# Kernel tuning notes

Hardware: AMD Instinct MI355X
Metric: run time of the kernel (lower is better)

The kernel has to match this reference:

```python
import jax, jax.numpy as jnp
import numpy as np

E = 1024
H = 16
CH = E // H

def setup_inputs() -> dict:
    key = jax.random.key(0)
    ks = jax.random.split(key, 9)
    s = E ** -0.5
    return {
        'x': jax.random.normal(ks[0], (4, 2048, E), dtype=jnp.float32),
        'Wq': jax.random.normal(ks[1], (E, E), dtype=jnp.float32) * s,
        'bq': jnp.zeros((E,), dtype=jnp.float32),
        'Wk': jax.random.normal(ks[2], (E, E), dtype=jnp.float32) * s,
        'bk': jnp.zeros((E,), dtype=jnp.float32),
        'Wv': jax.random.normal(ks[3], (E, E), dtype=jnp.float32) * s,
        'bv': jnp.zeros((E,), dtype=jnp.float32),
        'Wo': jax.random.normal(ks[4], (E, E), dtype=jnp.float32) * s,
        'bo': jnp.zeros((E,), dtype=jnp.float32),
    }

def _split_heads(t):
    # [..., n, H*ch] -> [..., H, n, ch]
    b, n, e = t.shape
    return t.reshape(b, n, H, CH).transpose(0, 2, 1, 3)

def reference(x, Wq, bq, Wk, bk, Wv, bv, Wo, bo):
    scale = CH ** -0.5
    q = _split_heads(x @ Wq.T + bq)  # [b,H,n,ch]
    k = _split_heads(x @ Wk.T + bk)
    v = _split_heads(x @ Wv.T + bv)
    att = jnp.einsum('bhqc,bhkc->bhqk', q, k) * scale
    att = jax.nn.softmax(att, axis=-1)
    out = jnp.einsum('bhqk,bhkc->bhqc', att, v)  # [b,H,n,ch]
    b, h, n, c = out.shape
    out = out.transpose(0, 2, 1, 3).reshape(b, n, h * c)
    return out @ Wo.T + bo
```

## Files before the change

### kernel.cpp

```cpp
#include <hip/hip_runtime.h>
#include <stdint.h>

#define EMB   1024
#define NHEAD 16
#define CHD   64
#define NB    4
#define SEQ   2048
#define NTOK  (NB * SEQ)
#define KDIM  1024

typedef __attribute__((ext_vector_type(8))) short  bf16x8;
typedef __attribute__((ext_vector_type(4))) short  short4v;
typedef __attribute__((ext_vector_type(4))) float  f32x4;
typedef __attribute__((ext_vector_type(4))) float  float4v;

__device__ __forceinline__ short f2bf(float f) {
    unsigned int u = __float_as_uint(f);
    u += 0x7fffu + ((u >> 16) & 1u);
    return (short)(u >> 16);
}

__device__ __forceinline__ void async16(const short* g, short* l) {
    __builtin_amdgcn_global_load_lds((__attribute__((address_space(1))) void const*)g,
                                     (__attribute__((address_space(3))) void*)l, 16, 0, 0);
}

__global__ __launch_bounds__(256) void cvt_all(const float* __restrict__ x,
                                               const float* __restrict__ Wq,
                                               const float* __restrict__ Wk,
                                               const float* __restrict__ Wv,
                                               const float* __restrict__ Wo,
                                               short* __restrict__ xb,
                                               short* __restrict__ Wqb,
                                               short* __restrict__ Wkb,
                                               short* __restrict__ Wvb,
                                               short* __restrict__ Wob) {
    int bid = blockIdx.x;
    const float* src;
    short* dst;
    int idx;
    if (bid < 8192) {
        src = x; dst = xb; idx = bid * 256 + threadIdx.x;
    } else {
        int w  = (bid - 8192) >> 10;
        int lb = (bid - 8192) & 1023;
        src = (w == 0) ? Wq : (w == 1) ? Wk : (w == 2) ? Wv : Wo;
        dst = (w == 0) ? Wqb : (w == 1) ? Wkb : (w == 2) ? Wvb : Wob;
        idx = lb * 256 + threadIdx.x;
    }
    float4v v = ((const float4v*)src)[idx];
    short4v s;
    s.x = f2bf(v.x); s.y = f2bf(v.y); s.z = f2bf(v.z); s.w = f2bf(v.w);
    ((short4v*)dst)[idx] = s;
}

__device__ __forceinline__ void gemm_core(const short* __restrict__ Atile,
                                          const short* __restrict__ Btile,
                                          short* As, short* Bs, f32x4 acc[4][4]) {
    const int tid  = threadIdx.x;
    const int wave = tid >> 6, lane = tid & 63;
    const int quad = lane >> 4, l16 = lane & 15;
    const int wm = (wave >> 1) * 64, wn = (wave & 1) * 64;
    const int srow = lane >> 2;
    const int scol = (lane & 3) * 8;

    for (int k0 = 0; k0 < KDIM; k0 += 32) {
        __syncthreads();
#pragma unroll
        for (int c = 0; c < 2; ++c) {
            int chunk = wave * 2 + c;
            int row = chunk * 16 + srow;
            async16(Atile + (size_t)row * KDIM + k0 + scol, As + chunk * 512);
            async16(Btile + (size_t)row * KDIM + k0 + scol, Bs + chunk * 512);
        }
        __syncthreads();
        bf16x8 af[4], bfr[4];
#pragma unroll
        for (int i = 0; i < 4; ++i)
            af[i] = *(const bf16x8*)&As[(wm + i * 16 + l16) * 32 + quad * 8];
#pragma unroll
        for (int j = 0; j < 4; ++j)
            bfr[j] = *(const bf16x8*)&Bs[(wn + j * 16 + l16) * 32 + quad * 8];
#pragma unroll
        for (int i = 0; i < 4; ++i)
#pragma unroll
            for (int j = 0; j < 4; ++j)
                acc[i][j] = __builtin_amdgcn_mfma_f32_16x16x32_bf16(af[i], bfr[j], acc[i][j], 0, 0, 0);
    }
}

#define QSCALE 0.1803368801111204f


#define MFMA16(A,B,C) __builtin_amdgcn_mfma_f32_16x16x32_bf16(A,B,C,0,0,0)
#define BARR  { __builtin_amdgcn_s_barrier(); __builtin_amdgcn_sched_barrier(0); }
#define VMC4  asm volatile("s_waitcnt vmcnt(4)" ::: "memory");
#define VMC0  asm volatile("s_waitcnt vmcnt(0)" ::: "memory");
#define PRIO1 __builtin_amdgcn_s_setprio(1);
#define PRIO0 __builtin_amdgcn_s_setprio(0);

#define STAGE_A_(BUF,H,T) { \
    async16(aS0 + (size_t)(H)*131072 + (T)*64, sm + (BUF)*32768 + (H)*8192 + stA); \
    async16(aS1 + (size_t)(H)*131072 + (T)*64, sm + (BUF)*32768 + (H)*8192 + 4096 + stA); }
#define STAGE_B_(BUF,H,T) { \
    async16(bS0 + (size_t)(H)*131072 + (T)*64, sm + (BUF)*32768 + 16384 + (H)*8192 + stA); \
    async16(bS1 + (size_t)(H)*131072 + (T)*64, sm + (BUF)*32768 + 16384 + (H)*8192 + 4096 + stA); }

#define LDB_(BUF) { \
    const short* _pb = sm + (BUF)*32768 + bro; \
    bfr[0][0] = *(const bf16x8*)(_pb + ac0);        bfr[0][1] = *(const bf16x8*)(_pb + ac1); \
    bfr[1][0] = *(const bf16x8*)(_pb + 1024 + ac0); bfr[1][1] = *(const bf16x8*)(_pb + 1024 + ac1); \
    bfr[2][0] = *(const bf16x8*)(_pb + 2048 + ac0); bfr[2][1] = *(const bf16x8*)(_pb + 2048 + ac1); \
    bfr[3][0] = *(const bf16x8*)(_pb + 3072 + ac0); bfr[3][1] = *(const bf16x8*)(_pb + 3072 + ac1); }

#define LDA_(BUF,Q) { \
    const short* _pa = sm + (BUF)*32768 + aro + (Q)*2048; \
    af[0][0] = *(const bf16x8*)(_pa + ac0);        af[0][1] = *(const bf16x8*)(_pa + ac1); \
    af[1][0] = *(const bf16x8*)(_pa + 1024 + ac0); af[1][1] = *(const bf16x8*)(_pa + 1024 + ac1); }

#define MF_(Q) { \
    acc[2*(Q)][0]   = MFMA16(af[0][0], bfr[0][0], acc[2*(Q)][0]); \
    acc[2*(Q)][0]   = MFMA16(af[0][1], bfr[0][1], acc[2*(Q)][0]); \
    acc[2*(Q)][1]   = MFMA16(af[0][0], bfr[1][0], acc[2*(Q)][1]); \
    acc[2*(Q)][1]   = MFMA16(af[0][1], bfr[1][1], acc[2*(Q)][1]); \
    acc[2*(Q)][2]   = MFMA16(af[0][0], bfr[2][0], acc[2*(Q)][2]); \
    acc[2*(Q)][2]   = MFMA16(af[0][1], bfr[2][1], acc[2*(Q)][2]); \
    acc[2*(Q)][3]   = MFMA16(af[0][0], bfr[3][0], acc[2*(Q)][3]); \
    acc[2*(Q)][3]   = MFMA16(af[0][1], bfr[3][1], acc[2*(Q)][3]); \
    acc[2*(Q)+1][0] = MFMA16(af[1][0], bfr[0][0], acc[2*(Q)+1][0]); \
    acc[2*(Q)+1][0] = MFMA16(af[1][1], bfr[0][1], acc[2*(Q)+1][0]); \
    acc[2*(Q)+1][1] = MFMA16(af[1][0], bfr[1][0], acc[2*(Q)+1][1]); \
    acc[2*(Q)+1][1] = MFMA16(af[1][1], bfr[1][1], acc[2*(Q)+1][1]); \
    acc[2*(Q)+1][2] = MFMA16(af[1][0], bfr[2][0], acc[2*(Q)+1][2]); \
    acc[2*(Q)+1][2] = MFMA16(af[1][1], bfr[2][1], acc[2*(Q)+1][2]); \
    acc[2*(Q)+1][3] = MFMA16(af[1][0], bfr[3][0], acc[2*(Q)+1][3]); \
    acc[2*(Q)+1][3] = MFMA16(af[1][1], bfr[3][1], acc[2*(Q)+1][3]); }

#define WINDOW(RB, AB, TA, BB, TB) \
    LDB_(RB) LDA_(RB,0) STAGE_A_(AB,0,TA) BARR \
    PRIO1 MF_(0) PRIO0 BARR \
    LDA_(RB,1) STAGE_A_(AB,1,TA) BARR \
    PRIO1 MF_(1) PRIO0 BARR \
    LDA_(RB,2) STAGE_B_(BB,0,TB) BARR \
    PRIO1 MF_(2) PRIO0 BARR \
    LDA_(RB,3) STAGE_B_(BB,1,TB) BARR \
    PRIO1 MF_(3) PRIO0 VMC4 BARR

__global__ __launch_bounds__(512, 2) void qk256(const short* __restrict__ xb,
                                                const short* __restrict__ Wqk,
                                                const float* __restrict__ bq,
                                                const float* __restrict__ bk,
                                                short* __restrict__ Qb,
                                                short* __restrict__ Kb) {
    extern __shared__ short sm[];
    const int bm = blockIdx.x, bn = blockIdx.y;
    const int tid = threadIdx.x;
    const int w = tid >> 6, lane = tid & 63;
    const int kq = lane >> 4, l16 = lane & 15;
    const int wmi = w >> 2, wni = w & 3;

    const int colsw = ((lane & 7) * 8) ^ (((lane >> 5) & 1) << 4);
    const short* aS0 = xb  + (size_t)(bm * 256 + w * 8 + (lane >> 3)) * 1024 + colsw;
    const short* aS1 = aS0 + (size_t)64 * 1024;
    const short* bS0 = Wqk + (size_t)(bn * 256 + w * 8 + (lane >> 3)) * 1024 + colsw;
    const short* bS1 = bS0 + (size_t)64 * 1024;
    const int stA = w * 512;

    const int swz = (l16 & 4) ? 16 : 0;
    const int ac0 = (kq * 8) ^ swz;
    const int ac1 = (32 + kq * 8) ^ swz;
    const int aro = wmi * 8192 + l16 * 64;
    const int bro = 16384 + (wni >> 1) * 8192 + ((wni & 1) * 64 + l16) * 64;

    f32x4 acc[8][4];
    const f32x4 z = {0.f, 0.f, 0.f, 0.f};
#pragma unroll
    for (int m = 0; m < 8; ++m)
#pragma unroll
        for (int n = 0; n < 4; ++n) acc[m][n] = z;
    bf16x8 bfr[4][2], af[2][2];

    STAGE_A_(0,0,0) STAGE_A_(0,1,0) STAGE_B_(0,0,0) STAGE_B_(0,1,0)
    STAGE_B_(1,0,1) STAGE_B_(1,1,1)
    VMC4 BARR

    for (int it = 0; it < 7; ++it) {
        const int te = 2 * it;
        WINDOW(0, 1, te + 1, 0, te + 2)
        WINDOW(1, 0, te + 2, 1, te + 3)
    }
    LDB_(0) LDA_(0,0) STAGE_A_(1,0,15) BARR
    PRIO1 MF_(0) PRIO0 BARR
    LDA_(0,1) STAGE_A_(1,1,15) BARR
    PRIO1 MF_(1) PRIO0 BARR
    LDA_(0,2) BARR
    PRIO1 MF_(2) PRIO0 BARR
    LDA_(0,3) BARR
    PRIO1 MF_(3) PRIO0 VMC0 BARR
    LDB_(1)
    LDA_(1,0) MF_(0)
    LDA_(1,1) MF_(1)
    LDA_(1,2) MF_(2)
    LDA_(1,3) MF_(3)

    const bool isQ = (bn < 4);
    const float* bias = isQ ? bq : bk;
    short* dst = isQ ? Qb : Kb;
    const float sc = isQ ? QSCALE : 1.0f;
    const int fb = (bn & 3) * 256 + wni * 64 + l16;
    const int tok0 = bm * 256 + wmi * 128 + kq * 4;
#pragma unroll
    for (int n = 0; n < 4; ++n) {
        const int e = fb + n * 16;
        const int hh = e >> 6, cc = e & 63;
        const float bv_ = bias[e];
#pragma unroll
        for (int m = 0; m < 8; ++m)
#pragma unroll
            for (int r = 0; r < 4; ++r) {
                const int tok = tok0 + m * 16 + r;
                const int bb = tok >> 11, nn = tok & 2047;
                dst[(((size_t)bb * NHEAD + hh) * SEQ + nn) * CHD + cc] =
                    f2bf((acc[m][n][r] + bv_) * sc);
            }
    }
}

__global__ __launch_bounds__(256) void vproj(const short* __restrict__ xb,
                                             const short* __restrict__ Wvb,
                                             const float* __restrict__ bv,
                                             short* __restrict__ Vtb) {
    __shared__ short As[128 * 32], Bs[128 * 32];
    const int bm = blockIdx.x;
    const int ew = blockIdx.y * 128;

    f32x4 acc[4][4];
    const f32x4 z = {0.f, 0.f, 0.f, 0.f};
#pragma unroll
    for (int i = 0; i < 4; ++i)
#pragma unroll
        for (int j = 0; j < 4; ++j) acc[i][j] = z;

    gemm_core(Wvb + (size_t)ew * KDIM, xb + (size_t)bm * 128 * KDIM, As, Bs, acc);

    const int lane = threadIdx.x & 63, wave = threadIdx.x >> 6;
    const int quad = lane >> 4, l16 = lane & 15;
    const int wm = (wave >> 1) * 64, wn = (wave & 1) * 64;
#pragma unroll
    for (int i = 0; i < 4; ++i)
#pragma unroll
        for (int j = 0; j < 4; ++j)
#pragma unroll
            for (int r = 0; r < 4; ++r) {
                int e = ew + wm + i * 16 + quad * 4 + r;
                int token = bm * 128 + wn + j * 16 + l16;
                int bb = token >> 11, nn = token & 2047;
                int hh = e >> 6, cc = e & 63;
                Vtb[(((size_t)bb * NHEAD + hh) * CHD + cc) * SEQ + nn] =
                    f2bf(acc[i][j][r] + bv[e]);
            }
}

__global__ __launch_bounds__(256, 4) void attn(const short* __restrict__ Qb,
                                               const short* __restrict__ Kb,
                                               const short* __restrict__ Vtb,
                                               short* __restrict__ AOb) {
    __shared__ short Ks[16 * 512];
    __shared__ short Vs[16 * 512];

    const int lid = blockIdx.x;
    const int bh = (lid & 7) * 8 + (lid >> 7);
    const int qt = (lid >> 3) & 15;

    const int tid = threadIdx.x, wave = tid >> 6, lane = tid & 63;
    const int quad = lane >> 4, l16 = lane & 15;

    const short* Kg = Kb  + (size_t)bh * SEQ * CHD;
    const short* Vg = Vtb + (size_t)bh * CHD * SEQ;

    bf16x8 qf0[2], qf1[2];
#pragma unroll
    for (int g = 0; g < 2; ++g) {
        const short* Qg = Qb + ((size_t)bh * SEQ + qt * 128 + wave * 32 + g * 16 + l16) * CHD;
        qf0[g] = *(const bf16x8*)(Qg + quad * 8);
        qf1[g] = *(const bf16x8*)(Qg + 32 + quad * 8);
    }

    const int kr = lane >> 3, ku = (lane & 7) ^ kr;
    const int vr = lane >> 4, vu = (lane & 15) ^ (vr << 2);

    int koff[4], voff[4];
#pragma unroll
    for (int cc = 0; cc < 4; ++cc) {
        int c = wave * 4 + cc;
        int l = c * 8 + kr;
        int j = l >> 4, m = l & 15;
        int kvg = ((j >> 1) << 5) + ((m >> 2) << 3) + ((j & 1) << 2) + (m & 3);
        koff[cc] = kvg * CHD + ku * 8;
        voff[cc] = (c * 4 + vr) * SEQ + vu * 8;
    }

    const int krow = l16 & 7;
    const int kbase = ((l16 >> 3) * 512) + krow * 64;
    const short* kp0 = Ks + kbase + ((quad ^ krow) << 3);
    const short* kp1 = Ks + kbase + (((4 + quad) ^ krow) << 3);
    const int vrow = l16 & 3;
    const short* vp = Vs + (l16 >> 2) * 512 + vrow * 128 + quad * 8;

    const f32x4 zf = {0.f, 0.f, 0.f, 0.f};
    const bf16x8 onesv = {16256, 16256, 16256, 16256, 16256, 16256, 16256, 16256};
    f32x4 O[2][4];
#pragma unroll
    for (int g = 0; g < 2; ++g)
#pragma unroll
        for (int nb = 0; nb < 4; ++nb) O[g][nb] = zf;
    f32x4 lacc[2];
    lacc[0] = zf; lacc[1] = zf;

    const short* Kgp = Kg;
    const short* Vgp = Vg;

    for (int kt = 0; kt < 16; ++kt) {
        __syncthreads();
#pragma unroll
        for (int cc = 0; cc < 4; ++cc) {
            int c = wave * 4 + cc;
            async16(Kgp + koff[cc], Ks + c * 512);
            async16(Vgp + voff[cc], Vs + c * 512);
        }
        Kgp += 128 * CHD;
        Vgp += 128;
        __syncthreads();

#pragma unroll
        for (int kk = 0; kk < 4; ++kk) {
            bf16x8 kA0 = *(const bf16x8*)(kp0 + (2 * kk) * 1024);
            bf16x8 kA1 = *(const bf16x8*)(kp1 + (2 * kk) * 1024);
            bf16x8 kB0 = *(const bf16x8*)(kp0 + (2 * kk + 1) * 1024);
            bf16x8 kB1 = *(const bf16x8*)(kp1 + (2 * kk + 1) * 1024);

            union { int i[4]; bf16x8 v; } pf[2];
#pragma unroll
            for (int g = 0; g < 2; ++g) {
                PRIO1
                f32x4 sA = __builtin_amdgcn_mfma_f32_16x16x32_bf16(kA0, qf0[g], zf, 0, 0, 0);
                sA = __builtin_amdgcn_mfma_f32_16x16x32_bf16(kA1, qf1[g], sA, 0, 0, 0);
                f32x4 sB = __builtin_amdgcn_mfma_f32_16x16x32_bf16(kB0, qf0[g], zf, 0, 0, 0);
                sB = __builtin_amdgcn_mfma_f32_16x16x32_bf16(kB1, qf1[g], sB, 0, 0, 0);
                PRIO0

                unsigned a0 = __float_as_uint(__builtin_amdgcn_exp2f(sA.x));
                unsigned a1 = __float_as_uint(__builtin_amdgcn_exp2f(sA.y));
                unsigned a2 = __float_as_uint(__builtin_amdgcn_exp2f(sA.z));
                unsigned a3 = __float_as_uint(__builtin_amdgcn_exp2f(sA.w));
                unsigned b0 = __float_as_uint(__builtin_amdgcn_exp2f(sB.x));
                unsigned b1 = __float_as_uint(__builtin_amdgcn_exp2f(sB.y));
                unsigned b2 = __float_as_uint(__builtin_amdgcn_exp2f(sB.z));
                unsigned b3 = __float_as_uint(__builtin_amdgcn_exp2f(sB.w));
                pf[g].i[0] = __builtin_amdgcn_perm(a1, a0, 0x07060302u);
                pf[g].i[1] = __builtin_amdgcn_perm(a3, a2, 0x07060302u);
                pf[g].i[2] = __builtin_amdgcn_perm(b1, b0, 0x07060302u);
                pf[g].i[3] = __builtin_amdgcn_perm(b3, b2, 0x07060302u);

                lacc[g] = __builtin_amdgcn_mfma_f32_16x16x32_bf16(pf[g].v, onesv, lacc[g], 0, 0, 0);
            }

            const short* vpk = vp + ((kk ^ vrow) << 5);
            PRIO1
#pragma unroll
            for (int nb = 0; nb < 4; ++nb) {
                bf16x8 vf = *(const bf16x8*)(vpk + nb * 2048);
#pragma unroll
                for (int g = 0; g < 2; ++g)
                    O[g][nb] = __builtin_amdgcn_mfma_f32_16x16x32_bf16(pf[g].v, vf, O[g][nb], 0, 0, 0);
            }
            PRIO0
        }
    }

    const int b = bh >> 4, h = bh & 15;
#pragma unroll
    for (int g = 0; g < 2; ++g) {
        float linv[4];
#pragma unroll
        for (int r = 0; r < 4; ++r) linv[r] = 1.0f / lacc[g][r];
#pragma unroll
        for (int nb = 0; nb < 4; ++nb)
#pragma unroll
            for (int r = 0; r < 4; ++r) {
                int n = qt * 128 + wave * 32 + g * 16 + quad * 4 + r;
                int cc = nb * 16 + l16;
                AOb[((size_t)b * SEQ + n) * EMB + h * CHD + cc] = f2bf(O[g][nb][r] * linv[r]);
            }
    }
}

__global__ __launch_bounds__(256) void out_gemm(const short* __restrict__ AOb,
                                                const short* __restrict__ Wob,
                                                const float* __restrict__ bo,
                                                float* __restrict__ out) {
    __shared__ short As[128 * 32], Bs[128 * 32];
    const int bm = blockIdx.x, bn = blockIdx.y;

    f32x4 acc[4][4];
    const f32x4 z = {0.f, 0.f, 0.f, 0.f};
#pragma unroll
    for (int i = 0; i < 4; ++i)
#pragma unroll
        for (int j = 0; j < 4; ++j) acc[i][j] = z;

    gemm_core(AOb + (size_t)bm * 128 * KDIM, Wob + (size_t)bn * 128 * KDIM, As, Bs, acc);

    const int lane = threadIdx.x & 63, wave = threadIdx.x >> 6;
    const int quad = lane >> 4, l16 = lane & 15;
    const int wm = (wave >> 1) * 64, wn = (wave & 1) * 64;
#pragma unroll
    for (int i = 0; i < 4; ++i)
#pragma unroll
        for (int j = 0; j < 4; ++j)
#pragma unroll
            for (int r = 0; r < 4; ++r) {
                int token = bm * 128 + wm + i * 16 + quad * 4 + r;
                int e = bn * 128 + wn + j * 16 + l16;
                out[(size_t)token * EMB + e] = acc[i][j][r] + bo[e];
            }
}

extern "C" void kernel_launch(void* const* d_in, const int* in_sizes, int n_in,
                              void* d_out, int out_size, void* d_ws, size_t ws_size,
                              hipStream_t stream) {
    const float* x  = (const float*)d_in[0];
    const float* Wq = (const float*)d_in[1];
    const float* bq = (const float*)d_in[2];
    const float* Wk = (const float*)d_in[3];
    const float* bk = (const float*)d_in[4];
    const float* Wv = (const float*)d_in[5];
    const float* bv = (const float*)d_in[6];
    const float* Wo = (const float*)d_in[7];
    const float* bo = (const float*)d_in[8];

    char* ws = (char*)d_ws;
    short* xb  = (short*)(ws + 0);
    short* Wqb = (short*)(ws + (size_t)16 * 1024 * 1024);
    short* Wkb = (short*)(ws + (size_t)18 * 1024 * 1024);
    short* Wvb = (short*)(ws + (size_t)20 * 1024 * 1024);
    short* Wob = (short*)(ws + (size_t)22 * 1024 * 1024);
    short* Qb  = (short*)(ws + (size_t)24 * 1024 * 1024);
    short* Kb  = (short*)(ws + (size_t)40 * 1024 * 1024);
    short* Vtb = (short*)(ws + (size_t)56 * 1024 * 1024);
    short* AOb = (short*)(ws + (size_t)72 * 1024 * 1024);

    static bool s_cfg = false;
    if (!s_cfg) {
        hipFuncSetAttribute(reinterpret_cast<const void*>(qk256),
                            hipFuncAttributeMaxDynamicSharedMemorySize, 131072);
        s_cfg = true;
    }

    cvt_all<<<dim3(8192 + 4096), dim3(256), 0, stream>>>(x, Wq, Wk, Wv, Wo,
                                                         xb, Wqb, Wkb, Wvb, Wob);
    qk256<<<dim3(32, 8), dim3(512), 131072, stream>>>(xb, Wqb, bq, bk, Qb, Kb);
    vproj<<<dim3(64, 8), dim3(256), 0, stream>>>(xb, Wvb, bv, Vtb);
    attn<<<dim3(1024), dim3(256), 0, stream>>>(Qb, Kb, Vtb, AOb);
    out_gemm<<<dim3(64, 8), dim3(256), 0, stream>>>(AOb, Wob, bo, (float*)d_out);
}
```

Measured before the change: 262.7 us.

## Replace V-projection and output GEMMs with pipelined 256x128 swizzled MFMA kernels

Replaces the simple single-buffered 128x128 GEMM used by the V projection and the output projection with a 256x128 tile, 512-thread kernel. The new kernel double-buffers K-tiles of 64 in dynamic LDS, using async global-to-LDS loads with XOR-swizzled columns, partial vmcnt waits and setprio around MFMA bursts. The aim is to overlap loads with compute, cut LDS bank conflicts and raise data reuse in these two GEMMs. The cost is a larger LDS footprint (96KB per block), which limits occupancy, and a more fragile hand-scheduled pipeline.

```diff
diff --git a/kernel.cpp b/kernel.cpp
--- a/kernel.cpp
+++ b/kernel.cpp
@@ -24,6 +24,14 @@
     __builtin_amdgcn_global_load_lds((__attribute__((address_space(1))) void const*)g,
                                      (__attribute__((address_space(3))) void*)l, 16, 0, 0);
 }
+
+#define MFMA16(A,B,C) __builtin_amdgcn_mfma_f32_16x16x32_bf16(A,B,C,0,0,0)
+#define BARR  { __builtin_amdgcn_s_barrier(); __builtin_amdgcn_sched_barrier(0); }
+#define VMC4  asm volatile("s_waitcnt vmcnt(4)" ::: "memory");
+#define VMC2  asm volatile("s_waitcnt vmcnt(2)" ::: "memory");
+#define VMC0  asm volatile("s_waitcnt vmcnt(0)" ::: "memory");
+#define PRIO1 __builtin_amdgcn_s_setprio(1);
+#define PRIO0 __builtin_amdgcn_s_setprio(0);
 
 __global__ __launch_bounds__(256) void cvt_all(const float* __restrict__ x,
                                                const float* __restrict__ Wq,
@@ -54,50 +62,8 @@
     ((short4v*)dst)[idx] = s;
 }
 
-__device__ __forceinline__ void gemm_core(const short* __restrict__ Atile,
-                                          const short* __restrict__ Btile,
-                                          short* As, short* Bs, f32x4 acc[4][4]) {
-    const int tid  = threadIdx.x;
-    const int wave = tid >> 6, lane = tid & 63;
-    const int quad = lane >> 4, l16 = lane & 15;
-    const int wm = (wave >> 1) * 64, wn = (wave & 1) * 64;
-    const int srow = lane >> 2;
-    const int scol = (lane & 3) * 8;
-
-    for (int k0 = 0; k0 < KDIM; k0 += 32) {
-        __syncthreads();
-#pragma unroll
-        for (int c = 0; c < 2; ++c) {
-            int chunk = wave * 2 + c;
-            int row = chunk * 16 + srow;
-            async16(Atile + (size_t)row * KDIM + k0 + scol, As + chunk * 512);
-            async16(Btile + (size_t)row * KDIM + k0 + scol, Bs + chunk * 512);
-        }
-        __syncthreads();
-        bf16x8 af[4], bfr[4];
-#pragma unroll
-        for (int i = 0; i < 4; ++i)
-            af[i] = *(const bf16x8*)&As[(wm + i * 16 + l16) * 32 + quad * 8];
-#pragma unroll
-        for (int j = 0; j < 4; ++j)
-            bfr[j] = *(const bf16x8*)&Bs[(wn + j * 16 + l16) * 32 + quad * 8];
-#pragma unroll
-        for (int i = 0; i < 4; ++i)
-#pragma unroll
-            for (int j = 0; j < 4; ++j)
-                acc[i][j] = __builtin_amdgcn_mfma_f32_16x16x32_bf16(af[i], bfr[j], acc[i][j], 0, 0, 0);
-    }
-}
-
 #define QSCALE 0.1803368801111204f
 
-
-#define MFMA16(A,B,C) __builtin_amdgcn_mfma_f32_16x16x32_bf16(A,B,C,0,0,0)
-#define BARR  { __builtin_amdgcn_s_barrier(); __builtin_amdgcn_sched_barrier(0); }
-#define VMC4  asm volatile("s_waitcnt vmcnt(4)" ::: "memory");
-#define VMC0  asm volatile("s_waitcnt vmcnt(0)" ::: "memory");
-#define PRIO1 __builtin_amdgcn_s_setprio(1);
-#define PRIO0 __builtin_amdgcn_s_setprio(0);
 
 #define STAGE_A_(BUF,H,T) { \
     async16(aS0 + (size_t)(H)*131072 + (T)*64, sm + (BUF)*32768 + (H)*8192 + stA); \
@@ -226,39 +192,166 @@
     }
 }
 
-__global__ __launch_bounds__(256) void vproj(const short* __restrict__ xb,
-                                             const short* __restrict__ Wvb,
-                                             const float* __restrict__ bv,
-                                             short* __restrict__ Vtb) {
-    __shared__ short As[128 * 32], Bs[128 * 32];
-    const int bm = blockIdx.x;
-    const int ew = blockIdx.y * 128;
-
-    f32x4 acc[4][4];
+
+#define SA3_(BUF,H,T) { \
+    async16(aS0 + (size_t)(H)*131072 + (T)*64, sm + (BUF)*24576 + (H)*8192 + stA); \
+    async16(aS1 + (size_t)(H)*131072 + (T)*64, sm + (BUF)*24576 + (H)*8192 + 4096 + stA); }
+#define SB3_(BUF,T) { \
+    async16(bS0 + (size_t)(T)*64, sm + (BUF)*24576 + 16384 + stA); \
+    async16(bS1 + (size_t)(T)*64, sm + (BUF)*24576 + 16384 + 4096 + stA); }
+
+#define LB3_(BUF) { \
+    const short* _pb = sm + (BUF)*24576 + bro; \
+    bfr[0][0] = *(const bf16x8*)(_pb + ac0);        bfr[0][1] = *(const bf16x8*)(_pb + ac1); \
+    bfr[1][0] = *(const bf16x8*)(_pb + 1024 + ac0); bfr[1][1] = *(const bf16x8*)(_pb + 1024 + ac1); }
+
+#define LA3_(BUF,Q) { \
+    const short* _pa = sm + (BUF)*24576 + aro + (Q)*2048; \
+    af[0][0] = *(const bf16x8*)(_pa + ac0);        af[0][1] = *(const bf16x8*)(_pa + ac1); \
+    af[1][0] = *(const bf16x8*)(_pa + 1024 + ac0); af[1][1] = *(const bf16x8*)(_pa + 1024 + ac1); }
+
+#define MF3_(Q) { \
+    acc[2*(Q)][0]   = MFMA16(af[0][0], bfr[0][0], acc[2*(Q)][0]); \
+    acc[2*(Q)][0]   = MFMA16(af[0][1], bfr[0][1], acc[2*(Q)][0]); \
+    acc[2*(Q)][1]   = MFMA16(af[0][0], bfr[1][0], acc[2*(Q)][1]); \
+    acc[2*(Q)][1]   = MFMA16(af[0][1], bfr[1][1], acc[2*(Q)][1]); \
+    acc[2*(Q)+1][0] = MFMA16(af[1][0], bfr[0][0], acc[2*(Q)+1][0]); \
+    acc[2*(Q)+1][0] = MFMA16(af[1][1], bfr[0][1], acc[2*(Q)+1][0]); \
+    acc[2*(Q)+1][1] = MFMA16(af[1][0], bfr[1][0], acc[2*(Q)+1][1]); \
+    acc[2*(Q)+1][1] = MFMA16(af[1][1], bfr[1][1], acc[2*(Q)+1][1]); }
+
+#define WIN3(RB, AB, TA, BB, TB) \
+    LB3_(RB) LA3_(RB,0) SA3_(AB,0,TA) BARR \
+    PRIO1 MF3_(0) PRIO0 BARR \
+    LA3_(RB,1) SA3_(AB,1,TA) BARR \
+    PRIO1 MF3_(1) PRIO0 BARR \
+    LA3_(RB,2) SB3_(BB,TB) BARR \
+    PRIO1 MF3_(2) PRIO0 BARR \
+    LA3_(RB,3) BARR \
+    PRIO1 MF3_(3) PRIO0 VMC2 BARR
+
+__device__ __forceinline__ void g256x128_core(short* sm,
+        const short* aS0, const short* aS1,
+        const short* bS0, const short* bS1,
+        const int stA, const int ac0, const int ac1,
+        const int aro, const int bro, f32x4 acc[8][2]) {
     const f32x4 z = {0.f, 0.f, 0.f, 0.f};
 #pragma unroll
-    for (int i = 0; i < 4; ++i)
-#pragma unroll
-        for (int j = 0; j < 4; ++j) acc[i][j] = z;
-
-    gemm_core(Wvb + (size_t)ew * KDIM, xb + (size_t)bm * 128 * KDIM, As, Bs, acc);
-
-    const int lane = threadIdx.x & 63, wave = threadIdx.x >> 6;
-    const int quad = lane >> 4, l16 = lane & 15;
-    const int wm = (wave >> 1) * 64, wn = (wave & 1) * 64;
-#pragma unroll
-    for (int i = 0; i < 4; ++i)
-#pragma unroll
-        for (int j = 0; j < 4; ++j)
+    for (int m = 0; m < 8; ++m)
+#pragma unroll
+        for (int n = 0; n < 2; ++n) acc[m][n] = z;
+    bf16x8 bfr[2][2], af[2][2];
+
+    SA3_(0,0,0) SA3_(0,1,0) SB3_(0,0)
+    SB3_(1,1)
+    VMC2 BARR
+
+    for (int it = 0; it < 7; ++it) {
+        const int te = 2 * it;
+        WIN3(0, 1, te + 1, 0, te + 2)
+        WIN3(1, 0, te + 2, 1, te + 3)
+    }
+    LB3_(0) LA3_(0,0) SA3_(1,0,15) BARR
+    PRIO1 MF3_(0) PRIO0 BARR
+    LA3_(0,1) SA3_(1,1,15) BARR
+    PRIO1 MF3_(1) PRIO0 BARR
+    LA3_(0,2) BARR
+    PRIO1 MF3_(2) PRIO0 BARR
+    LA3_(0,3) BARR
+    PRIO1 MF3_(3) PRIO0 VMC0 BARR
+    LB3_(1)
+    LA3_(1,0) MF3_(0)
+    LA3_(1,1) MF3_(1)
+    LA3_(1,2) MF3_(2)
+    LA3_(1,3) MF3_(3)
+}
+
+__global__ __launch_bounds__(512, 2) void vproj256(const short* __restrict__ xb,
+                                                   const short* __restrict__ Wvb,
+                                                   const float* __restrict__ bv,
+                                                   short* __restrict__ Vtb) {
+    extern __shared__ short sm[];
+    const int bm = blockIdx.x, bn = blockIdx.y;
+    const int tid = threadIdx.x;
+    const int w = tid >> 6, lane = tid & 63;
+    const int kq = lane >> 4, l16 = lane & 15;
+    const int wmi = w >> 2, wni = w & 3;
+
+    const int colsw = ((lane & 7) * 8) ^ (((lane >> 5) & 1) << 4);
+    const short* aS0 = Wvb + (size_t)(bm * 256 + w * 8 + (lane >> 3)) * 1024 + colsw;
+    const short* aS1 = aS0 + (size_t)64 * 1024;
+    const short* bS0 = xb  + (size_t)(bn * 128 + w * 8 + (lane >> 3)) * 1024 + colsw;
+    const short* bS1 = bS0 + (size_t)64 * 1024;
+    const int stA = w * 512;
+
+    const int swz = (l16 & 4) ? 16 : 0;
+    const int ac0 = (kq * 8) ^ swz;
+    const int ac1 = (32 + kq * 8) ^ swz;
+    const int aro = wmi * 8192 + l16 * 64;
+    const int bro = 16384 + (wni * 32 + l16) * 64;
+
+    f32x4 acc[8][2];
+    g256x128_core(sm, aS0, aS1, bS0, bS1, stA, ac0, ac1, aro, bro, acc);
+
+    const int f0 = bm * 256 + wmi * 128 + kq * 4;
+    const int t0 = bn * 128 + wni * 32 + l16;
+#pragma unroll
+    for (int n = 0; n < 2; ++n) {
+        const int tok = t0 + n * 16;
+        const int bb = tok >> 11, nn = tok & 2047;
+#pragma unroll
+        for (int m = 0; m < 8; ++m)
 #pragma unroll
             for (int r = 0; r < 4; ++r) {
-                int e = ew + wm + i * 16 + quad * 4 + r;
-                int token = bm * 128 + wn + j * 16 + l16;
-                int bb = token >> 11, nn = token & 2047;
-                int hh = e >> 6, cc = e & 63;
+                const int e = f0 + m * 16 + r;
+                const int hh = e >> 6, cc = e & 63;
                 Vtb[(((size_t)bb * NHEAD + hh) * CHD + cc) * SEQ + nn] =
-                    f2bf(acc[i][j][r] + bv[e]);
+                    f2bf(acc[m][n][r] + bv[e]);
             }
+    }
+}
+
+__global__ __launch_bounds__(512, 2) void out256(const short* __restrict__ AOb,
+                                                 const short* __restrict__ Wob,
+                                                 const float* __restrict__ bo,
+                                                 float* __restrict__ out) {
+    extern __shared__ short sm[];
+    const int bm = blockIdx.x, bn = blockIdx.y;
+    const int tid = threadIdx.x;
+    const int w = tid >> 6, lane = tid & 63;
+    const int kq = lane >> 4, l16 = lane & 15;
+    const int wmi = w >> 2, wni = w & 3;
+
+    const int colsw = ((lane & 7) * 8) ^ (((lane >> 5) & 1) << 4);
+    const short* aS0 = AOb + (size_t)(bm * 256 + w * 8 + (lane >> 3)) * 1024 + colsw;
+    const short* aS1 = aS0 + (size_t)64 * 1024;
+    const short* bS0 = Wob + (size_t)(bn * 128 + w * 8 + (lane >> 3)) * 1024 + colsw;
+    const short* bS1 = bS0 + (size_t)64 * 1024;
+    const int stA = w * 512;
+
+    const int swz = (l16 & 4) ? 16 : 0;
+    const int ac0 = (kq * 8) ^ swz;
+    const int ac1 = (32 + kq * 8) ^ swz;
+    const int aro = wmi * 8192 + l16 * 64;
+    const int bro = 16384 + (wni * 32 + l16) * 64;
+
+    f32x4 acc[8][2];
+    g256x128_core(sm, aS0, aS1, bS0, bS1, stA, ac0, ac1, aro, bro, acc);
+
+    const int tok0 = bm * 256 + wmi * 128 + kq * 4;
+    const int e0   = bn * 128 + wni * 32 + l16;
+#pragma unroll
+    for (int n = 0; n < 2; ++n) {
+        const int e = e0 + n * 16;
+        const float bo_ = bo[e];
+#pragma unroll
+        for (int m = 0; m < 8; ++m)
+#pragma unroll
+            for (int r = 0; r < 4; ++r) {
+                const int tok = tok0 + m * 16 + r;
+                out[(size_t)tok * EMB + e] = acc[m][n][r] + bo_;
+            }
+    }
 }
 
 __global__ __launch_bounds__(256, 4) void attn(const short* __restrict__ Qb,
@@ -395,37 +488,6 @@
     }
 }
 
-__global__ __launch_bounds__(256) void out_gemm(const short* __restrict__ AOb,
-                                                const short* __restrict__ Wob,
-                                                const float* __restrict__ bo,
-                                                float* __restrict__ out) {
-    __shared__ short As[128 * 32], Bs[128 * 32];
-    const int bm = blockIdx.x, bn = blockIdx.y;
-
-    f32x4 acc[4][4];
-    const f32x4 z = {0.f, 0.f, 0.f, 0.f};
-#pragma unroll
-    for (int i = 0; i < 4; ++i)
-#pragma unroll
-        for (int j = 0; j < 4; ++j) acc[i][j] = z;
-
-    gemm_core(AOb + (size_t)bm * 128 * KDIM, Wob + (size_t)bn * 128 * KDIM, As, Bs, acc);
-
-    const int lane = threadIdx.x & 63, wave = threadIdx.x >> 6;
-    const int quad = lane >> 4, l16 = lane & 15;
-    const int wm = (wave >> 1) * 64, wn = (wave & 1) * 64;
-#pragma unroll
-    for (int i = 0; i < 4; ++i)
-#pragma unroll
-        for (int j = 0; j < 4; ++j)
-#pragma unroll
-            for (int r = 0; r < 4; ++r) {
-                int token = bm * 128 + wm + i * 16 + quad * 4 + r;
-                int e = bn * 128 + wn + j * 16 + l16;
-                out[(size_t)token * EMB + e] = acc[i][j][r] + bo[e];
-            }
-}
-
 extern "C" void kernel_launch(void* const* d_in, const int* in_sizes, int n_in,
                               void* d_out, int out_size, void* d_ws, size_t ws_size,
                               hipStream_t stream) {
@@ -454,13 +516,17 @@
     if (!s_cfg) {
         hipFuncSetAttribute(reinterpret_cast<const void*>(qk256),
                             hipFuncAttributeMaxDynamicSharedMemorySize, 131072);
+        hipFuncSetAttribute(reinterpret_cast<const void*>(vproj256),
+                            hipFuncAttributeMaxDynamicSharedMemorySize, 98304);
+        hipFuncSetAttribute(reinterpret_cast<const void*>(out256),
+                            hipFuncAttributeMaxDynamicSharedMemorySize, 98304);
         s_cfg = true;
     }
 
     cvt_all<<<dim3(8192 + 4096), dim3(256), 0, stream>>>(x, Wq, Wk, Wv, Wo,
                                                          xb, Wqb, Wkb, Wvb, Wob);
     qk256<<<dim3(32, 8), dim3(512), 131072, stream>>>(xb, Wqb, bq, bk, Qb, Kb);
-    vproj<<<dim3(64, 8), dim3(256), 0, stream>>>(xb, Wvb, bv, Vtb);
+    vproj256<<<dim3(4, 64), dim3(512), 98304, stream>>>(xb, Wvb, bv, Vtb);
     attn<<<dim3(1024), dim3(256), 0, stream>>>(Qb, Kb, Vtb, AOb);
-    out_gemm<<<dim3(64, 8), dim3(256), 0, stream>>>(AOb, Wob, bo, (float*)d_out);
-}
+    out256<<<dim3(32, 8), dim3(512), 98304, stream>>>(AOb, Wob, bo, (float*)d_out);
+}
```

Measured after the change: 263.5 us. Within noise of the previous version (+0.3%).
